# Kernel optimization log

Measured on AMD Instinct MI355X. Metric: run time of the kernel, lower is better.

Reference implementation:

```python
import jax, jax.numpy as jnp
import numpy as np

S1 = (42, 1600, 1408); S2 = (21, 800, 704); S3 = (11, 400, 352); S4 = (6, 200, 176)
OFF = np.array([[dz, dy, dx] for dz in (-1, 0, 1) for dy in (-1, 0, 1) for dx in (-1, 0, 1)], np.int64)
KOFF = np.array([[kz, ky, kx] for kz in (0, 1, 2) for ky in (0, 1, 2) for kx in (0, 1, 2)], np.int64)

def _keys(c, s):
    return (c[:, 0] * s[1] + c[:, 1]) * s[2] + c[:, 2]

def _lookup(skeys, qk, valid):
    pos = np.searchsorted(skeys, qk)
    posc = np.clip(pos, 0, len(skeys) - 1)
    found = valid & (skeys[posc] == qk)
    return np.where(found, posc, -1).astype(np.int32)

def _subm_nbr(coords, skeys, shape):
    N = len(coords); nbr = np.empty((N, 27), np.int32); sh = np.array(shape)
    for t in range(27):
        q = coords + OFF[t]
        valid = np.all((q >= 0) & (q < sh), axis=1)
        nbr[:, t] = _lookup(skeys, _keys(q, shape), valid)
    return nbr

def _inv_nbr(fcoords, ckeys, cshape):
    # inverse of stride-2, pad-1, k-3 sparse conv: coarse = (fine + 1 - k) / 2
    N = len(fcoords); nbr = np.empty((N, 27), np.int32); csh = np.array(cshape)
    for t in range(27):
        cand = fcoords + 1 - KOFF[t]
        valid = np.all(cand >= 0, axis=1) & np.all(cand % 2 == 0, axis=1)
        cc = cand // 2
        valid &= np.all(cc < csh, axis=1)
        nbr[:, t] = _lookup(ckeys, _keys(cc, cshape), valid)
    return nbr

def _geometry():
    rng = np.random.default_rng(0)
    n = 130000
    c = np.stack([rng.integers(0, S1[i], n) for i in range(3)], 1).astype(np.int64)
    uk, idx = np.unique(_keys(c, S1), return_index=True)
    c1 = c[idx][:100000]; k1 = uk[:len(c1)]
    def down(cf, s):
        cc = cf // 2
        uk, idx = np.unique(_keys(cc, s), return_index=True)
        return cc[idx], uk
    c2, k2 = down(c1, S2); c3, k3 = down(c2, S3); c4, k4 = down(c3, S4)
    return dict(nbr4=_subm_nbr(c4, k4, S4), inv43=_inv_nbr(c3, k4, S4),
                nbr3=_subm_nbr(c3, k3, S3), inv32=_inv_nbr(c2, k3, S3),
                nbr2=_subm_nbr(c2, k2, S2), inv21=_inv_nbr(c1, k2, S2),
                nbr1=_subm_nbr(c1, k1, S1), n4=len(c4), n1=len(c1))

_SPECS = [("m4", 64, 64), ("i4", 64, 64), ("m3", 64, 64), ("i3", 64, 32),
          ("m2", 32, 32), ("i2", 32, 16), ("m1", 16, 16), ("c5", 16, 3)]

def _params(key):
    p = {}
    for i, (nm, ci, co) in enumerate(_SPECS):
        k = jax.random.fold_in(key, i)
        p["W_" + nm] = jax.random.normal(k, (27, ci, co), jnp.float32) * (1.0 / np.sqrt(27.0 * ci))
        p["g_" + nm] = jnp.ones((co,), jnp.float32)
        p["b_" + nm] = jnp.zeros((co,), jnp.float32)
    return p

def setup_inputs() -> dict:
    geo = _geometry()
    key = jax.random.key(0)
    inp = {k: jnp.asarray(v) for k, v in geo.items() if k.startswith(("nbr", "inv"))}
    inp["x"] = jax.random.normal(jax.random.fold_in(key, 100), (geo["n4"], 64), jnp.float32)
    inp.update(_params(key))
    return inp

def _block(f, nbr, W, g, b, relu=True):
    # gather-GEMM (sparse conv), then BatchNorm1d (training mode, eps=1e-3), then ReLU
    m = nbr >= 0                                             # [N,27]
    x = jnp.where(m[..., None], f[jnp.maximum(nbr, 0)], 0.0)  # [N,27,Cin]
    y = jnp.einsum('nkc,kcd->nd', x, W)                      # [N,Cout]
    mu = y.mean(0); var = y.var(0)
    y = (y - mu) * jax.lax.rsqrt(var + 1e-3) * g + b
    return jax.nn.relu(y) if relu else y

def reference(x, nbr4, inv43, nbr3, inv32, nbr2, inv21, nbr1,
              W_m4, g_m4, b_m4, W_i4, g_i4, b_i4, W_m3, g_m3, b_m3, W_i3, g_i3, b_i3,
              W_m2, g_m2, b_m2, W_i2, g_i2, b_i2, W_m1, g_m1, b_m1, W_c5, g_c5, b_c5):
    h = _block(x, nbr4, W_m4, g_m4, b_m4)      # subm4: [N4,64]
    h = _block(h, inv43, W_i4, g_i4, b_i4)     # inverse conv4 -> [N3,64]
    h = _block(h, nbr3, W_m3, g_m3, b_m3)      # subm3
    h = _block(h, inv32, W_i3, g_i3, b_i3)     # inverse conv3 -> [N2,32]
    h = _block(h, nbr2, W_m2, g_m2, b_m2)      # subm2
    h = _block(h, inv21, W_i2, g_i2, b_i2)     # inverse conv2 -> [N1,16]
    h = _block(h, nbr1, W_m1, g_m1, b_m1)      # subm1
    return _block(h, nbr1, W_c5, g_c5, b_c5, relu=False)  # conv5 (shares subm1 rulebook), BN only
```

## Files before the change

kernel.cpp:

```cpp
#include <hip/hip_runtime.h>

typedef _Float16 HALF;
typedef _Float16 f16x8 __attribute__((ext_vector_type(8)));
typedef float f32x4 __attribute__((ext_vector_type(4)));
typedef int i32x4 __attribute__((ext_vector_type(4)));

struct WArgs { const float* W[8]; HALF* dst[8]; };

__global__ void convert_all_w_kernel(WArgs a)
{
    const int CIs[8]  = {64, 64, 64, 64, 32, 32, 16, 16};
    const int COs[8]  = {64, 64, 64, 32, 32, 16, 16, 3};
    const int COPs[8] = {64, 64, 64, 32, 32, 16, 16, 16};
    const int L = blockIdx.y;
    const int CI = CIs[L], CO = COs[L], COP = COPs[L];
    const int K = 27 * CI, KP = (K + 31) & ~31;
    const int total = COP * KP;
    for (int i = blockIdx.x * 256 + threadIdx.x; i < total; i += gridDim.x * 256) {
        int jp = i / KP;
        int kp = i - jp * KP;
        float v = (jp < CO && kp < K) ? a.W[L][(size_t)kp * CO + jp] : 0.f;
        a.dst[L][((size_t)(kp >> 5) * COP + jp) * 32 + (kp & 31)] = (HALF)v;
    }
}

__global__ void convert_x_kernel(const float* __restrict__ x, HALF* __restrict__ xh, int total)
{
    int i = blockIdx.x * 256 + threadIdx.x;
    if (i < total) xh[i] = (HALF)x[i];
}

__global__ void bn_prep_kernel(const float* __restrict__ sums, const float* __restrict__ g,
                               const float* __restrict__ b, float invn, int CO, int COP,
                               float* __restrict__ scbi)
{
    const int c = threadIdx.x;
    if (c >= CO) return;
    float s = 0.f, q = 0.f;
#pragma unroll
    for (int k = 0; k < 8; ++k) { s += sums[k * 128 + c]; q += sums[k * 128 + COP + c]; }
    const float mu  = s * invn;
    const float var = q * invn - mu * mu;
    const float sc  = rsqrtf(var + 1e-3f) * g[c];
    scbi[c]       = sc;
    scbi[128 + c] = b[c] - mu * sc;
}

template<int CI, int CO_PAD, int NMT, bool FUSED>
__global__ __launch_bounds__(256, 2) void conv_kernel(
    const HALF* __restrict__ h, const int* __restrict__ nbr,
    const HALF* __restrict__ Wt, HALF* __restrict__ yout,
    float* __restrict__ sums, int n,
    const float* __restrict__ pscbi)
{
    constexpr int K    = 27 * CI;
    constexpr int KP   = (K + 31) & ~31;
    constexpr int NCH  = KP / 32;
    constexpr int NJB  = CO_PAD / 16;
    constexpr int NW   = 4;
    constexpr int CHK  = (NCH + NW - 1) / NW;
    constexpr int NCB  = (CI >= 64) ? 2 : 1;
    static_assert(NCB == 1 || (CHK & 1) == 0, "sc8 parity must stay compile-time");
    constexpr int LOG2CI = (CI == 64) ? 6 : ((CI == 32) ? 5 : 4);
    constexpr int ROWS  = 16 * NMT;
    constexpr int PAIRS = NMT * NJB;

    __shared__ f32x4 lred[2][PAIRS * 64];

    const int wv   = threadIdx.x >> 6;
    const int lane = threadIdx.x & 63;
    const int l15  = lane & 15;
    const int lq   = lane >> 4;

    int bid = blockIdx.x;
    {
        const int nwg = gridDim.x;
        const int q = nwg >> 3, r = nwg & 7;
        const int xcd = bid & 7, idx = bid >> 3;
        bid = (xcd < r ? xcd * (q + 1) : r * (q + 1) + (xcd - r) * q) + idx;
    }
    const int rowBase = bid * ROWS;

    f32x4 acc[NMT][NJB];
#pragma unroll
    for (int mt = 0; mt < NMT; ++mt)
#pragma unroll
        for (int jb = 0; jb < NJB; ++jb)
#pragma unroll
            for (int r = 0; r < 4; ++r) acc[mt][jb][r] = 0.f;

    int  nbo[NMT];
    bool rok[NMT];
#pragma unroll
    for (int mt = 0; mt < NMT; ++mt) {
        const int row = rowBase + mt * 16 + l15;
        rok[mt] = row < n;
        nbo[mt] = min(row, n - 1) * 27;
    }

    f16x8 sc8[NCB], bi8[NCB];
    if constexpr (FUSED) {
#pragma unroll
        for (int cb = 0; cb < NCB; ++cb) {
            const int c0 = cb * 32 + ((lq * 8) & (CI - 1));
#pragma unroll
            for (int j = 0; j < 8; ++j) {
                sc8[cb][j] = (HALF)pscbi[c0 + j];
                bi8[cb][j] = (HALF)pscbi[128 + c0 + j];
            }
        }
    }

    #define TAPOF(kc_) ((CI == 16) ? (2 * (kc_) + (lq >> 1)) : ((CI == 64) ? ((kc_) >> 1) : (kc_)))
    #define CHOF(kc_)  ((((kc_) * 32) + lq * 8) & (CI - 1))

    const int kc0 = wv * CHK;

    int   ipf[2][NMT];
    f16x8 apf[2][NMT];
#pragma unroll
    for (int p = 0; p < 2; ++p) {
        const int kc = kc0 + p;
#pragma unroll
        for (int mt = 0; mt < NMT; ++mt) {
            const int t   = TAPOF(kc);
            const int v   = nbr[nbo[mt] + (t < 27 ? t : 26)];
            const int idx = (rok[mt] && t < 27) ? v : -1;
            ipf[p][mt] = idx;
            apf[p][mt] = *(const f16x8*)(h + ((max(idx, 0) << LOG2CI) + CHOF(kc)));
        }
    }

#pragma unroll
    for (int kc2 = 0; kc2 < CHK; ++kc2) {
        const int kc = kc0 + kc2;
        if (kc >= NCH) break;
        const int cur = kc2 & 1;
        const int ccb = (NCB == 2) ? (kc2 & 1) : 0;

        const HALF* wb = Wt + (size_t)kc * (CO_PAD * 32) + lq * 8;
        f16x8 b[NJB];
#pragma unroll
        for (int jb = 0; jb < NJB; ++jb)
            b[jb] = *(const f16x8*)(wb + (size_t)(jb * 16 + l15) * 32);

        f16x8 a_use[NMT];
        int   i_use[NMT];
#pragma unroll
        for (int mt = 0; mt < NMT; ++mt) { a_use[mt] = apf[cur][mt]; i_use[mt] = ipf[cur][mt]; }

        if (kc2 + 2 < CHK && kc + 2 < NCH) {
#pragma unroll
            for (int mt = 0; mt < NMT; ++mt) {
                const int t   = TAPOF(kc + 2);
                const int v   = nbr[nbo[mt] + (t < 27 ? t : 26)];
                const int idx = (rok[mt] && t < 27) ? v : -1;
                ipf[cur][mt] = idx;
                apf[cur][mt] = *(const f16x8*)(h + ((max(idx, 0) << LOG2CI) + CHOF(kc + 2)));
            }
        }

#pragma unroll
        for (int mt = 0; mt < NMT; ++mt) {
            f16x8 a = a_use[mt];
            if constexpr (FUSED) {
                a = a * sc8[ccb] + bi8[ccb];
#pragma unroll
                for (int j = 0; j < 8; ++j)
                    a[j] = (a[j] < (HALF)0.f) ? (HALF)0.f : a[j];
            }
            const int m = ~(i_use[mt] >> 31);
            i32x4 ai = __builtin_bit_cast(i32x4, a);
            ai.x &= m; ai.y &= m; ai.z &= m; ai.w &= m;
            a = __builtin_bit_cast(f16x8, ai);
#pragma unroll
            for (int jb = 0; jb < NJB; ++jb)
                acc[mt][jb] = __builtin_amdgcn_mfma_f32_16x16x32_f16(a, b[jb], acc[mt][jb], 0, 0, 0);
        }
    }
    #undef TAPOF
    #undef CHOF

    if (wv & 1) {
#pragma unroll
        for (int mt = 0; mt < NMT; ++mt)
#pragma unroll
            for (int jb = 0; jb < NJB; ++jb)
                lred[wv >> 1][(mt * NJB + jb) * 64 + lane] = acc[mt][jb];
    }
    __syncthreads();
    if (!(wv & 1)) {
#pragma unroll
        for (int mt = 0; mt < NMT; ++mt)
#pragma unroll
            for (int jb = 0; jb < NJB; ++jb)
                acc[mt][jb] += lred[wv >> 1][(mt * NJB + jb) * 64 + lane];
    }
    __syncthreads();
    if (wv == 2) {
#pragma unroll
        for (int mt = 0; mt < NMT; ++mt)
#pragma unroll
            for (int jb = 0; jb < NJB; ++jb)
                lred[0][(mt * NJB + jb) * 64 + lane] = acc[mt][jb];
    }
    __syncthreads();

    if (wv == 0) {
#pragma unroll
        for (int mt = 0; mt < NMT; ++mt)
#pragma unroll
            for (int jb = 0; jb < NJB; ++jb)
                acc[mt][jb] += lred[0][(mt * NJB + jb) * 64 + lane];

        float* sl = sums + (bid & 7) * 128;
#pragma unroll
        for (int jb = 0; jb < NJB; ++jb) {
            const int col = jb * 16 + l15;
            float s = 0.f, sq = 0.f;
#pragma unroll
            for (int mt = 0; mt < NMT; ++mt) {
                const int rb = rowBase + mt * 16 + lq * 4;
#pragma unroll
                for (int r = 0; r < 4; ++r) {
                    if (rb + r < n) {
                        const float v = acc[mt][jb][r];
                        yout[(size_t)(rb + r) * CO_PAD + col] = (HALF)v;
                        s += v;
                        sq += v * v;
                    }
                }
            }
            s  += __shfl_xor(s, 16);  s  += __shfl_xor(s, 32);
            sq += __shfl_xor(sq, 16); sq += __shfl_xor(sq, 32);
            if (lane < 16) {
                atomicAdd(&sl[col], s);
                atomicAdd(&sl[CO_PAD + col], sq);
            }
        }
    }
}

__global__ void bn_out_kernel(const HALF* __restrict__ y, const float* __restrict__ sums,
                              const float* __restrict__ g, const float* __restrict__ b,
                              int n, float invn, float* __restrict__ out)
{
    int i = blockIdx.x * 256 + threadIdx.x;
    if (i >= n * 3) return;
    int row = i / 3;
    int c = i - row * 3;
    float ssum = 0.f, qsum = 0.f;
#pragma unroll
    for (int k2 = 0; k2 < 8; ++k2) {
        ssum += sums[k2 * 128 + c];
        qsum += sums[k2 * 128 + 16 + c];
    }
    float mu  = ssum * invn;
    float var = qsum * invn - mu * mu;
    float sc  = rsqrtf(var + 1e-3f) * g[c];
    out[i] = ((float)y[(size_t)row * 16 + c] - mu) * sc + b[c];
}

extern "C" void kernel_launch(void* const* d_in, const int* in_sizes, int n_in,
                              void* d_out, int out_size, void* d_ws, size_t ws_size,
                              hipStream_t stream)
{
    const int* nbr4  = (const int*)d_in[0];
    const int* inv43 = (const int*)d_in[1];
    const int* nbr3  = (const int*)d_in[2];
    const int* inv32 = (const int*)d_in[3];
    const int* nbr2  = (const int*)d_in[4];
    const int* inv21 = (const int*)d_in[5];
    const int* nbr1  = (const int*)d_in[6];
    const float* x   = (const float*)d_in[7];

    const int n4 = in_sizes[0] / 27;
    const int n3 = in_sizes[1] / 27;
    const int n2 = in_sizes[3] / 27;
    const int n1 = in_sizes[5] / 27;

    const int CIs[8]  = {64, 64, 64, 64, 32, 32, 16, 16};
    const int COs[8]  = {64, 64, 64, 32, 32, 16, 16, 3};
    const int COPs[8] = {64, 64, 64, 32, 32, 16, 16, 16};
    int KPs[8], wtoff[8];
    int wtot = 0;
    for (int s = 0; s < 8; ++s) {
        KPs[s] = ((27 * CIs[s] + 31) / 32) * 32;
        wtoff[s] = wtot;
        wtot += COPs[s] * KPs[s];
    }

    char* ws = (char*)d_ws;
    HALF* wt = (HALF*)ws;
    size_t off = ((size_t)wtot * sizeof(HALF) + 255) & ~(size_t)255;
    float* sums = (float*)(ws + off);
    off += 8 * 1024 * sizeof(float);
    off = (off + 255) & ~(size_t)255;
    float* scbi = (float*)(ws + off);
    off += 8 * 256 * sizeof(float);
    off = (off + 255) & ~(size_t)255;
    HALF* xh = (HALF*)(ws + off);
    off += ((size_t)n4 * 64 * sizeof(HALF) + 255) & ~(size_t)255;
    size_t bufElems = 0;
    {
        size_t cand[4] = {(size_t)n4 * 64, (size_t)n3 * 64, (size_t)n2 * 32, (size_t)n1 * 16};
        for (int i = 0; i < 4; ++i) if (cand[i] > bufElems) bufElems = cand[i];
    }
    HALF* Y0 = (HALF*)(ws + off);
    off += (bufElems * sizeof(HALF) + 255) & ~(size_t)255;
    HALF* Y1 = (HALF*)(ws + off);

    hipMemsetAsync(sums, 0, 8 * 1024 * sizeof(float), stream);

    WArgs wa;
    for (int s = 0; s < 8; ++s) { wa.W[s] = (const float*)d_in[8 + 3 * s]; wa.dst[s] = wt + wtoff[s]; }
    {
        int maxTotal = 64 * KPs[0];
        dim3 grid((maxTotal + 255) / 256, 8);
        convert_all_w_kernel<<<grid, 256, 0, stream>>>(wa);
    }
    convert_x_kernel<<<(n4 * 64 + 255) / 256, 256, 0, stream>>>(x, xh, n4 * 64);

#define G(s) ((const float*)d_in[9 + 3 * (s)])
#define B(s) ((const float*)d_in[10 + 3 * (s)])
#define SUMS(s) (sums + (s) * 1024)
#define SCBI(s) (scbi + (s) * 256)
#define GRID(nn) (((nn) + 31) / 32)
#define PREP(s, invn) bn_prep_kernel<<<1, 128, 0, stream>>>(SUMS(s), G(s), B(s), (invn), COs[s], COPs[s], SCBI(s))

    conv_kernel<64, 64, 2, false><<<GRID(n4), 256, 0, stream>>>(
        xh, nbr4, wt + wtoff[0], Y0, SUMS(0), n4, nullptr);
    PREP(0, 1.f / n4);
    conv_kernel<64, 64, 2, true><<<GRID(n3), 256, 0, stream>>>(
        Y0, inv43, wt + wtoff[1], Y1, SUMS(1), n3, SCBI(0));
    PREP(1, 1.f / n3);
    conv_kernel<64, 64, 2, true><<<GRID(n3), 256, 0, stream>>>(
        Y1, nbr3, wt + wtoff[2], Y0, SUMS(2), n3, SCBI(1));
    PREP(2, 1.f / n3);
    conv_kernel<64, 32, 2, true><<<GRID(n2), 256, 0, stream>>>(
        Y0, inv32, wt + wtoff[3], Y1, SUMS(3), n2, SCBI(2));
    PREP(3, 1.f / n2);
    conv_kernel<32, 32, 2, true><<<GRID(n2), 256, 0, stream>>>(
        Y1, nbr2, wt + wtoff[4], Y0, SUMS(4), n2, SCBI(3));
    PREP(4, 1.f / n2);
    conv_kernel<32, 16, 2, true><<<GRID(n1), 256, 0, stream>>>(
        Y0, inv21, wt + wtoff[5], Y1, SUMS(5), n1, SCBI(4));
    PREP(5, 1.f / n1);
    conv_kernel<16, 16, 2, true><<<GRID(n1), 256, 0, stream>>>(
        Y1, nbr1, wt + wtoff[6], Y0, SUMS(6), n1, SCBI(5));
    PREP(6, 1.f / n1);
    conv_kernel<16, 16, 2, true><<<GRID(n1), 256, 0, stream>>>(
        Y0, nbr1, wt + wtoff[7], Y1, SUMS(7), n1, SCBI(6));
    bn_out_kernel<<<(n1 * 3 + 255) / 256, 256, 0, stream>>>(
        Y1, SUMS(7), G(7), B(7), n1, 1.f / n1, (float*)d_out);

#undef G
#undef B
#undef SUMS
#undef SCBI
#undef GRID
#undef PREP
}
```

Measured before the change: 517.5 us.

## Split conv work across waves by output columns and rows instead of K-chunks

Each wave now handles the full K reduction for one 16-column output slice and a 32-row group, instead of a K-split across four waves. This removes the LDS cross-wave reduction and its three block barriers. It also uses nontemporal loads for weights and nontemporal stores for outputs. In exchange, each wave runs a longer serial K loop, and waves sharing rows re-gather the same neighbor features, so gather traffic goes up when WC>1.

```diff
diff --git a/kernel.cpp b/kernel.cpp
--- a/kernel.cpp
+++ b/kernel.cpp
@@ -46,31 +46,29 @@
     scbi[128 + c] = b[c] - mu * sc;
 }
 
-template<int CI, int CO_PAD, int NMT, bool FUSED>
+template<int CI, int CO_PAD, int WC, bool FUSED>
 __global__ __launch_bounds__(256, 2) void conv_kernel(
     const HALF* __restrict__ h, const int* __restrict__ nbr,
     const HALF* __restrict__ Wt, HALF* __restrict__ yout,
     float* __restrict__ sums, int n,
     const float* __restrict__ pscbi)
 {
+    constexpr int NMT  = 2;
     constexpr int K    = 27 * CI;
     constexpr int KP   = (K + 31) & ~31;
     constexpr int NCH  = KP / 32;
-    constexpr int NJB  = CO_PAD / 16;
-    constexpr int NW   = 4;
-    constexpr int CHK  = (NCH + NW - 1) / NW;
+    constexpr int WR   = 4 / WC;
+    constexpr int ROWS = WR * 32;
+    constexpr int LWC  = (WC == 4) ? 2 : ((WC == 2) ? 1 : 0);
     constexpr int NCB  = (CI >= 64) ? 2 : 1;
-    static_assert(NCB == 1 || (CHK & 1) == 0, "sc8 parity must stay compile-time");
     constexpr int LOG2CI = (CI == 64) ? 6 : ((CI == 32) ? 5 : 4);
-    constexpr int ROWS  = 16 * NMT;
-    constexpr int PAIRS = NMT * NJB;
-
-    __shared__ f32x4 lred[2][PAIRS * 64];
 
     const int wv   = threadIdx.x >> 6;
     const int lane = threadIdx.x & 63;
     const int l15  = lane & 15;
     const int lq   = lane >> 4;
+    const int wc   = wv & (WC - 1);
+    const int wr   = wv >> LWC;
 
     int bid = blockIdx.x;
     {
@@ -79,15 +77,14 @@
         const int xcd = bid & 7, idx = bid >> 3;
         bid = (xcd < r ? xcd * (q + 1) : r * (q + 1) + (xcd - r) * q) + idx;
     }
-    const int rowBase = bid * ROWS;
-
-    f32x4 acc[NMT][NJB];
+    const int rowBase = bid * ROWS + wr * 32;
+    const int co0     = wc * 16;
+
+    f32x4 acc[NMT];
 #pragma unroll
     for (int mt = 0; mt < NMT; ++mt)
 #pragma unroll
-        for (int jb = 0; jb < NJB; ++jb)
-#pragma unroll
-            for (int r = 0; r < 4; ++r) acc[mt][jb][r] = 0.f;
+        for (int r = 0; r < 4; ++r) acc[mt][r] = 0.f;
 
     int  nbo[NMT];
     bool rok[NMT];
@@ -114,42 +111,34 @@
     #define TAPOF(kc_) ((CI == 16) ? (2 * (kc_) + (lq >> 1)) : ((CI == 64) ? ((kc_) >> 1) : (kc_)))
     #define CHOF(kc_)  ((((kc_) * 32) + lq * 8) & (CI - 1))
 
-    const int kc0 = wv * CHK;
-
     int   ipf[2][NMT];
     f16x8 apf[2][NMT];
 #pragma unroll
     for (int p = 0; p < 2; ++p) {
-        const int kc = kc0 + p;
 #pragma unroll
         for (int mt = 0; mt < NMT; ++mt) {
-            const int t   = TAPOF(kc);
+            const int t   = TAPOF(p);
             const int v   = nbr[nbo[mt] + (t < 27 ? t : 26)];
             const int idx = (rok[mt] && t < 27) ? v : -1;
             ipf[p][mt] = idx;
-            apf[p][mt] = *(const f16x8*)(h + ((max(idx, 0) << LOG2CI) + CHOF(kc)));
-        }
-    }
-
-#pragma unroll
-    for (int kc2 = 0; kc2 < CHK; ++kc2) {
-        const int kc = kc0 + kc2;
-        if (kc >= NCH) break;
-        const int cur = kc2 & 1;
-        const int ccb = (NCB == 2) ? (kc2 & 1) : 0;
-
-        const HALF* wb = Wt + (size_t)kc * (CO_PAD * 32) + lq * 8;
-        f16x8 b[NJB];
-#pragma unroll
-        for (int jb = 0; jb < NJB; ++jb)
-            b[jb] = *(const f16x8*)(wb + (size_t)(jb * 16 + l15) * 32);
+            apf[p][mt] = *(const f16x8*)(h + ((max(idx, 0) << LOG2CI) + CHOF(p)));
+        }
+    }
+
+#pragma unroll
+    for (int kc = 0; kc < NCH; ++kc) {
+        const int cur = kc & 1;
+        const int ccb = (NCB == 2) ? (kc & 1) : 0;
+
+        const HALF* wb = Wt + (size_t)kc * (CO_PAD * 32) + (size_t)(co0 + l15) * 32 + lq * 8;
+        const f16x8 b = __builtin_nontemporal_load((const f16x8*)wb);
 
         f16x8 a_use[NMT];
         int   i_use[NMT];
 #pragma unroll
         for (int mt = 0; mt < NMT; ++mt) { a_use[mt] = apf[cur][mt]; i_use[mt] = ipf[cur][mt]; }
 
-        if (kc2 + 2 < CHK && kc + 2 < NCH) {
+        if (kc + 2 < NCH) {
 #pragma unroll
             for (int mt = 0; mt < NMT; ++mt) {
                 const int t   = TAPOF(kc + 2);
@@ -173,71 +162,33 @@
             i32x4 ai = __builtin_bit_cast(i32x4, a);
             ai.x &= m; ai.y &= m; ai.z &= m; ai.w &= m;
             a = __builtin_bit_cast(f16x8, ai);
-#pragma unroll
-            for (int jb = 0; jb < NJB; ++jb)
-                acc[mt][jb] = __builtin_amdgcn_mfma_f32_16x16x32_f16(a, b[jb], acc[mt][jb], 0, 0, 0);
+            acc[mt] = __builtin_amdgcn_mfma_f32_16x16x32_f16(a, b, acc[mt], 0, 0, 0);
         }
     }
     #undef TAPOF
     #undef CHOF
 
-    if (wv & 1) {
-#pragma unroll
-        for (int mt = 0; mt < NMT; ++mt)
-#pragma unroll
-            for (int jb = 0; jb < NJB; ++jb)
-                lred[wv >> 1][(mt * NJB + jb) * 64 + lane] = acc[mt][jb];
-    }
-    __syncthreads();
-    if (!(wv & 1)) {
-#pragma unroll
-        for (int mt = 0; mt < NMT; ++mt)
-#pragma unroll
-            for (int jb = 0; jb < NJB; ++jb)
-                acc[mt][jb] += lred[wv >> 1][(mt * NJB + jb) * 64 + lane];
-    }
-    __syncthreads();
-    if (wv == 2) {
-#pragma unroll
-        for (int mt = 0; mt < NMT; ++mt)
-#pragma unroll
-            for (int jb = 0; jb < NJB; ++jb)
-                lred[0][(mt * NJB + jb) * 64 + lane] = acc[mt][jb];
-    }
-    __syncthreads();
-
-    if (wv == 0) {
-#pragma unroll
-        for (int mt = 0; mt < NMT; ++mt)
-#pragma unroll
-            for (int jb = 0; jb < NJB; ++jb)
-                acc[mt][jb] += lred[0][(mt * NJB + jb) * 64 + lane];
-
-        float* sl = sums + (bid & 7) * 128;
-#pragma unroll
-        for (int jb = 0; jb < NJB; ++jb) {
-            const int col = jb * 16 + l15;
-            float s = 0.f, sq = 0.f;
-#pragma unroll
-            for (int mt = 0; mt < NMT; ++mt) {
-                const int rb = rowBase + mt * 16 + lq * 4;
-#pragma unroll
-                for (int r = 0; r < 4; ++r) {
-                    if (rb + r < n) {
-                        const float v = acc[mt][jb][r];
-                        yout[(size_t)(rb + r) * CO_PAD + col] = (HALF)v;
-                        s += v;
-                        sq += v * v;
-                    }
-                }
+    float* sl = sums + (bid & 7) * 128;
+    const int col = co0 + l15;
+    float s = 0.f, sq = 0.f;
+#pragma unroll
+    for (int mt = 0; mt < NMT; ++mt) {
+        const int rb = rowBase + mt * 16 + lq * 4;
+#pragma unroll
+        for (int r = 0; r < 4; ++r) {
+            if (rb + r < n) {
+                const float v = acc[mt][r];
+                __builtin_nontemporal_store((HALF)v, &yout[(size_t)(rb + r) * CO_PAD + col]);
+                s += v;
+                sq += v * v;
             }
-            s  += __shfl_xor(s, 16);  s  += __shfl_xor(s, 32);
-            sq += __shfl_xor(sq, 16); sq += __shfl_xor(sq, 32);
-            if (lane < 16) {
-                atomicAdd(&sl[col], s);
-                atomicAdd(&sl[CO_PAD + col], sq);
-            }
-        }
+        }
+    }
+    s  += __shfl_xor(s, 16);  s  += __shfl_xor(s, 32);
+    sq += __shfl_xor(sq, 16); sq += __shfl_xor(sq, 32);
+    if (lane < 16) {
+        atomicAdd(&sl[col], s);
+        atomicAdd(&sl[CO_PAD + col], sq);
     }
 }
 
@@ -325,31 +276,31 @@
 #define B(s) ((const float*)d_in[10 + 3 * (s)])
 #define SUMS(s) (sums + (s) * 1024)
 #define SCBI(s) (scbi + (s) * 256)
-#define GRID(nn) (((nn) + 31) / 32)
+#define GRIDR(nn, rows) (((nn) + (rows) - 1) / (rows))
 #define PREP(s, invn) bn_prep_kernel<<<1, 128, 0, stream>>>(SUMS(s), G(s), B(s), (invn), COs[s], COPs[s], SCBI(s))
 
-    conv_kernel<64, 64, 2, false><<<GRID(n4), 256, 0, stream>>>(
+    conv_kernel<64, 64, 4, false><<<GRIDR(n4, 32), 256, 0, stream>>>(
         xh, nbr4, wt + wtoff[0], Y0, SUMS(0), n4, nullptr);
     PREP(0, 1.f / n4);
-    conv_kernel<64, 64, 2, true><<<GRID(n3), 256, 0, stream>>>(
+    conv_kernel<64, 64, 4, true><<<GRIDR(n3, 32), 256, 0, stream>>>(
         Y0, inv43, wt + wtoff[1], Y1, SUMS(1), n3, SCBI(0));
     PREP(1, 1.f / n3);
-    conv_kernel<64, 64, 2, true><<<GRID(n3), 256, 0, stream>>>(
+    conv_kernel<64, 64, 4, true><<<GRIDR(n3, 32), 256, 0, stream>>>(
         Y1, nbr3, wt + wtoff[2], Y0, SUMS(2), n3, SCBI(1));
     PREP(2, 1.f / n3);
-    conv_kernel<64, 32, 2, true><<<GRID(n2), 256, 0, stream>>>(
+    conv_kernel<64, 32, 2, true><<<GRIDR(n2, 64), 256, 0, stream>>>(
         Y0, inv32, wt + wtoff[3], Y1, SUMS(3), n2, SCBI(2));
     PREP(3, 1.f / n2);
-    conv_kernel<32, 32, 2, true><<<GRID(n2), 256, 0, stream>>>(
+    conv_kernel<32, 32, 2, true><<<GRIDR(n2, 64), 256, 0, stream>>>(
         Y1, nbr2, wt + wtoff[4], Y0, SUMS(4), n2, SCBI(3));
     PREP(4, 1.f / n2);
-    conv_kernel<32, 16, 2, true><<<GRID(n1), 256, 0, stream>>>(
+    conv_kernel<32, 16, 1, true><<<GRIDR(n1, 128), 256, 0, stream>>>(
         Y0, inv21, wt + wtoff[5], Y1, SUMS(5), n1, SCBI(4));
     PREP(5, 1.f / n1);
-    conv_kernel<16, 16, 2, true><<<GRID(n1), 256, 0, stream>>>(
+    conv_kernel<16, 16, 1, true><<<GRIDR(n1, 128), 256, 0, stream>>>(
         Y1, nbr1, wt + wtoff[6], Y0, SUMS(6), n1, SCBI(5));
     PREP(6, 1.f / n1);
-    conv_kernel<16, 16, 2, true><<<GRID(n1), 256, 0, stream>>>(
+    conv_kernel<16, 16, 1, true><<<GRIDR(n1, 128), 256, 0, stream>>>(
         Y0, nbr1, wt + wtoff[7], Y1, SUMS(7), n1, SCBI(6));
     bn_out_kernel<<<(n1 * 3 + 255) / 256, 256, 0, stream>>>(
         Y1, SUMS(7), G(7), B(7), n1, 1.f / n1, (float*)d_out);
@@ -358,6 +309,6 @@
 #undef B
 #undef SUMS
 #undef SCBI
-#undef GRID
+#undef GRIDR
 #undef PREP
 }
```

Result: slower. 766.6 us (+48.1%).
